# Kernel tuning notes

Measured on AMD Instinct MI355X. Metric: run time of the kernel, lower is better.

## Reference

```python
import jax, jax.numpy as jnp
import numpy as np

B, S, H = 2, 2048, 2048
NH, HD = 16, 128
I = 8192
EPS = float(np.finfo(np.float32).eps)  # torch RMSNorm default eps=None -> dtype eps


def rmsnorm(x, w):
    var = jnp.mean(jnp.square(x), axis=-1, keepdims=True)
    return x * jax.lax.rsqrt(var + EPS) * w


def setup_inputs() -> dict:
    key = jax.random.key(0)
    ks = jax.random.split(key, 8)
    s = 0.02
    return {
        "hidden_states": jax.random.normal(ks[0], (B, S, H), jnp.float32),
        "Wq": jax.random.normal(ks[1], (H, H), jnp.float32) * s,
        "Wk": jax.random.normal(ks[2], (H, H), jnp.float32) * s,
        "Wv": jax.random.normal(ks[3], (H, H), jnp.float32) * s,
        "Wo": jax.random.normal(ks[4], (H, H), jnp.float32) * s,
        "Wg": jax.random.normal(ks[5], (I, H), jnp.float32) * s,
        "Wu": jax.random.normal(ks[6], (I, H), jnp.float32) * s,
        "Wd": jax.random.normal(ks[7], (H, I), jnp.float32) * s,
        "g_in": jnp.ones((H,), jnp.float32),
        "g_post": jnp.ones((H,), jnp.float32),
    }


def reference(hidden_states, Wq, Wk, Wv, Wo, Wg, Wu, Wd, g_in, g_post):
    residual = hidden_states
    x = rmsnorm(hidden_states, g_in)
    # projections: nn.Linear does x @ W.T
    q = (x @ Wq.T).reshape(B, S, NH, HD).transpose(0, 2, 1, 3)  # [B,NH,S,HD]
    k = (x @ Wk.T).reshape(B, S, NH, HD).transpose(0, 2, 1, 3)
    v = (x @ Wv.T).reshape(B, S, NH, HD).transpose(0, 2, 1, 3)
    scores = jnp.einsum("bhqd,bhkd->bhqk", q, k) / jnp.sqrt(jnp.float32(HD))
    attn = jax.nn.softmax(scores, axis=-1)
    out = jnp.einsum("bhqk,bhkd->bhqd", attn, v)
    out = out.transpose(0, 2, 1, 3).reshape(B, S, H)
    hidden_states = residual + out @ Wo.T
    residual = hidden_states
    x = rmsnorm(hidden_states, g_post)
    mlp = (jax.nn.silu(x @ Wg.T) * (x @ Wu.T)) @ Wd.T
    return residual + mlp
```

## Files before the change

### kernel.cpp

```cpp
#include <hip/hip_runtime.h>

using u16 = unsigned short;
using u32 = unsigned int;

typedef __attribute__((ext_vector_type(8))) __bf16 bf16x8;
typedef __attribute__((ext_vector_type(4))) float f32x4;

__device__ __forceinline__ u16 f2bf(float f) {
  u32 u = __float_as_uint(f);
  u32 r = (u + 0x7fffu + ((u >> 16) & 1u)) >> 16;
  return (u16)r;
}
__device__ __forceinline__ u32 pk2(float a, float b) {
  return (u32)f2bf(a) | ((u32)f2bf(b) << 16);
}
__device__ __forceinline__ float bf2f(u16 h) {
  return __uint_as_float(((u32)h) << 16);
}
__device__ __forceinline__ void gload16(const u16* g, u16* l) {
  __builtin_amdgcn_global_load_lds((const __attribute__((address_space(1))) void*)g,
                                   (__attribute__((address_space(3))) void*)l, 16, 0, 0);
}
__device__ __forceinline__ f32x4 mfma_bf16(bf16x8 a, bf16x8 b, f32x4 c) {
  return __builtin_amdgcn_mfma_f32_16x16x32_bf16(a, b, c, 0, 0, 0);
}

__global__ __launch_bounds__(256) void cvt_bf16(const float* __restrict__ in,
                                                u16* __restrict__ out, int n8) {
  int i = blockIdx.x * 256 + threadIdx.x;
  int stride = gridDim.x * 256;
  for (; i < n8; i += stride) {
    float4 a = ((const float4*)in)[(size_t)i * 2];
    float4 b = ((const float4*)in)[(size_t)i * 2 + 1];
    ((uint4*)out)[i] = make_uint4(pk2(a.x, a.y), pk2(a.z, a.w), pk2(b.x, b.y), pk2(b.z, b.w));
  }
}

__global__ __launch_bounds__(256) void rmsnorm_bf16(const float* __restrict__ x,
                                                    const float* __restrict__ g,
                                                    u16* __restrict__ o) {
  const int row = blockIdx.x;
  const int tid = threadIdx.x;
  const float4* xr = (const float4*)(x + (size_t)row * 2048);
  float4 a = xr[tid * 2], b = xr[tid * 2 + 1];
  float s = a.x * a.x + a.y * a.y + a.z * a.z + a.w * a.w +
            b.x * b.x + b.y * b.y + b.z * b.z + b.w * b.w;
#pragma unroll
  for (int off = 1; off < 64; off <<= 1) s += __shfl_xor(s, off);
  __shared__ float red[4];
  if ((tid & 63) == 0) red[tid >> 6] = s;
  __syncthreads();
  s = red[0] + red[1] + red[2] + red[3];
  const float r = rsqrtf(s * (1.0f / 2048.0f) + 1.1920929e-07f);
  const float4* gr = (const float4*)g;
  float4 ga = gr[tid * 2], gb = gr[tid * 2 + 1];
  ((uint4*)(o + (size_t)row * 2048))[tid] =
      make_uint4(pk2(a.x * r * ga.x, a.y * r * ga.y), pk2(a.z * r * ga.z, a.w * r * ga.w),
                 pk2(b.x * r * gb.x, b.y * r * gb.y), pk2(b.z * r * gb.z, b.w * r * gb.w));
}

template <int EPI, int BN, int WM, int WN>
__global__ __launch_bounds__(512, 2) void gemm256(const u16* __restrict__ A,
                                                  const u16* __restrict__ B,
                                                  u16* Cb, float* Cf, const float* __restrict__ Res,
                                                  int M, int N, int K, int lda) {
  constexpr int NBH = BN / 128;
  constexpr int MR = 256 / WM / 16;
  constexpr int NR = BN / WN / 16;
  constexpr int HALF = 8192;
  alignas(16) __shared__ u16 lds[2][(2 + NBH) * HALF];

  const int tid = threadIdx.x;
  const int w = tid >> 6, lane = tid & 63;
  const int lo = lane & 15, hi = lane >> 4;

  const int nwg = gridDim.x;
  const int swz = (blockIdx.x & 7) * (nwg >> 3) + (blockIdx.x >> 3);
  const int nbx = N / BN;
  const int bm = (swz / nbx) * 256, bn = (swz % nbx) * BN;

  const int wm = w / WN, wn = w % WN;
  const int WRB = wm * (256 / WM), WCB = wn * (BN / WN);
  const int ah = WRB >> 7, arb = WRB & 127;
  const int bh = WCB >> 7, brb = WCB & 127;

  const int trow = tid >> 3, twin = tid & 7;
  const int scol = (twin ^ (trow & 7)) * 8;
  const u16* Ag = A + (size_t)(bm + trow) * lda + scol;
  const u16* Bg = B + (size_t)(bn + trow) * K + scol;

  f32x4 acc[MR][NR] = {};

#define STAGE(Ld, kt)                                                              \
  {                                                                                \
    _Pragma("unroll") for (int hc = 0; hc < 4; ++hc)                               \
        gload16(Ag + (size_t)(hc * 64) * lda + (kt), (Ld) + hc * 4096 + tid * 8);  \
    _Pragma("unroll") for (int hc = 0; hc < NBH * 2; ++hc)                         \
        gload16(Bg + (size_t)(hc * 64) * K + (kt), (Ld) + (2 + 0) * HALF + hc * 4096 + tid * 8); \
  }

  STAGE(&lds[0][0], 0);
  __syncthreads();
  int cur = 0;
  for (int kt = 0; kt < K; kt += 64) {
    if (kt + 64 < K) STAGE(&lds[cur ^ 1][0], kt + 64);
    const u16* LA = &lds[cur][0] + ah * HALF;
    const u16* LB = &lds[cur][0] + (2 + bh) * HALF;
#pragma unroll
    for (int ks = 0; ks < 2; ++ks) {
      const int pw = ((ks << 2) | hi) ^ (lo & 7);
      bf16x8 af[MR], bf[NR];
#pragma unroll
      for (int m = 0; m < MR; ++m)
        af[m] = *(const bf16x8*)(LA + (arb + m * 16 + lo) * 64 + pw * 8);
#pragma unroll
      for (int n = 0; n < NR; ++n)
        bf[n] = *(const bf16x8*)(LB + (brb + n * 16 + lo) * 64 + pw * 8);
      __builtin_amdgcn_s_setprio(1);
#pragma unroll
      for (int m = 0; m < MR; ++m)
#pragma unroll
        for (int n = 0; n < NR; ++n) acc[m][n] = mfma_bf16(af[m], bf[n], acc[m][n]);
      __builtin_amdgcn_s_setprio(0);
    }
    __syncthreads();
    cur ^= 1;
  }
#undef STAGE

#pragma unroll
  for (int m = 0; m < MR; ++m) {
    const int gr = bm + WRB + m * 16 + hi * 4;
#pragma unroll
    for (int n = 0; n < NR; ++n) {
      const int gc = bn + WCB + n * 16 + lo;
#pragma unroll
      for (int r = 0; r < 4; ++r) {
        const size_t idx = (size_t)(gr + r) * N + gc;
        if constexpr (EPI == 1) {
          Cf[idx] = Res[idx] + acc[m][n][r];
        } else if constexpr (EPI == 2) {
          float g = bf2f(Cb[idx]);
          float s = g / (1.f + __expf(-g));
          Cb[idx] = f2bf(s * acc[m][n][r]);
        } else {
          Cb[idx] = f2bf(acc[m][n][r]);
        }
      }
    }
  }
}

template <int EPI>
__global__ __launch_bounds__(256) void gemm_bt(const u16* __restrict__ A,
                                               const float* __restrict__ B,
                                               u16* Cb, float* Cf, const float* Res,
                                               int M, int N, int K) {
  alignas(16) __shared__ u16 As[128 * 32];
  alignas(16) __shared__ u16 Bs[128 * 32];
  const int tid = threadIdx.x;
  const int w = tid >> 6, lane = tid & 63;
  const int lo = lane & 15, hi = lane >> 4;
  const int bm = blockIdx.y * 128, bn = blockIdx.x * 128;
  const int wr = (w >> 1) * 64, wc = (w & 1) * 64;
  f32x4 acc[4][4] = {};
  const int r0 = tid >> 2, kc0 = (tid & 3) * 8;
  const u16* a0 = A + (size_t)(bm + r0) * K + kc0;
  const u16* a1 = A + (size_t)(bm + 64 + r0) * K + kc0;
  const float* b0 = B + (size_t)(bn + r0) * K + kc0;
  const float* b1 = B + (size_t)(bn + 64 + r0) * K + kc0;
  u16* asd0 = &As[(size_t)tid * 8];
  u16* asd1 = &As[(size_t)(tid + 256) * 8];
  u16* bsd0 = &Bs[(size_t)tid * 8];
  u16* bsd1 = &Bs[(size_t)(tid + 256) * 8];
  for (int kt = 0; kt < K; kt += 32) {
    gload16(a0 + kt, asd0);
    gload16(a1 + kt, asd1);
    float4 x0 = *(const float4*)(b0 + kt);
    float4 x1 = *(const float4*)(b0 + kt + 4);
    float4 y0 = *(const float4*)(b1 + kt);
    float4 y1 = *(const float4*)(b1 + kt + 4);
    *(uint4*)bsd0 = make_uint4(pk2(x0.x, x0.y), pk2(x0.z, x0.w), pk2(x1.x, x1.y), pk2(x1.z, x1.w));
    *(uint4*)bsd1 = make_uint4(pk2(y0.x, y0.y), pk2(y0.z, y0.w), pk2(y1.x, y1.y), pk2(y1.z, y1.w));
    __syncthreads();
    bf16x8 af[4], bfr[4];
#pragma unroll
    for (int i = 0; i < 4; ++i) {
      af[i] = *(const bf16x8*)(&As[(wr + i * 16 + lo) * 32 + hi * 8]);
      bfr[i] = *(const bf16x8*)(&Bs[(wc + i * 16 + lo) * 32 + hi * 8]);
    }
#pragma unroll
    for (int i = 0; i < 4; ++i)
#pragma unroll
      for (int j = 0; j < 4; ++j) acc[i][j] = mfma_bf16(af[i], bfr[j], acc[i][j]);
    __syncthreads();
  }
#pragma unroll
  for (int i = 0; i < 4; ++i) {
    const int gr = bm + wr + i * 16 + hi * 4;
#pragma unroll
    for (int j = 0; j < 4; ++j) {
      const int gc = bn + wc + j * 16 + lo;
#pragma unroll
      for (int r = 0; r < 4; ++r) {
        const size_t idx = (size_t)(gr + r) * N + gc;
        if constexpr (EPI == 1) {
          Cf[idx] = Res[idx] + acc[i][j][r];
        } else if constexpr (EPI == 2) {
          float g = bf2f(Cb[idx]);
          float s = g / (1.f + __expf(-g));
          Cb[idx] = f2bf(s * acc[i][j][r]);
        } else {
          Cb[idx] = f2bf(acc[i][j][r]);
        }
      }
    }
  }
}

__global__ __launch_bounds__(256) void transpose_v(const u16* __restrict__ v,
                                                   u16* __restrict__ vt, int ldv) {
  __shared__ u16 t[32][33];
  const int bh = blockIdx.z, b = bh >> 4, h = bh & 15;
  const int s0 = blockIdx.x * 32, d0 = blockIdx.y * 32;
  const int tx = threadIdx.x, ty = threadIdx.y;
#pragma unroll
  for (int i = 0; i < 4; ++i)
    t[ty + i * 8][tx] = v[(size_t)(b * 2048 + s0 + ty + i * 8) * ldv + h * 128 + d0 + tx];
  __syncthreads();
#pragma unroll
  for (int i = 0; i < 4; ++i)
    vt[(size_t)(bh * 128 + d0 + ty + i * 8) * 2048 + s0 + tx] = t[tx][ty + i * 8];
}

__global__ __launch_bounds__(256) void attn_fwd2(const u16* __restrict__ q,
                                                 const u16* __restrict__ k,
                                                 const u16* __restrict__ vt,
                                                 u16* o, int ldq) {
  constexpr int S = 2048;
  alignas(16) __shared__ u16 Ks[2][64 * 128];
  alignas(16) __shared__ u16 Vs[2][128 * 64];
  alignas(16) __shared__ u16 plds[4][16 * 72];
  const int bh = blockIdx.y, b = bh >> 4, h = bh & 15;
  const int tid = threadIdx.x, w = tid >> 6, lane = tid & 63;
  const int lo = lane & 15, hi = lane >> 4;
  const int qr = blockIdx.x * 64 + w * 16;
  u16* pl = &plds[w][0];

  bf16x8 qf[4];
  const u16* qb = q + (size_t)(b * S + qr + lo) * ldq + h * 128 + hi * 8;
#pragma unroll
  for (int ks = 0; ks < 4; ++ks) qf[ks] = *(const bf16x8*)(qb + ks * 32);

  f32x4 oacc[8] = {};
  float m[4], l[4];
#pragma unroll
  for (int r = 0; r < 4; ++r) { m[r] = -1e30f; l[r] = 0.f; }

  const u16* kb = k + (size_t)(b * S) * ldq + h * 128;
  const u16* vb = vt + (size_t)bh * 128 * S;

  const int kcs = ((((tid & 15) * 16) ^ (((tid >> 4) & 7) << 4)) >> 1);
  const int vcs = ((((tid & 7) * 16) ^ (((tid >> 3) & 7) << 4)) >> 1);
  const u16* kgs = kb + (size_t)(tid >> 4) * ldq + kcs;
  const u16* vgs = vb + (size_t)(tid >> 3) * S + vcs;

  int cur = 0;
#pragma unroll
  for (int c = 0; c < 4; ++c) gload16(kgs + (size_t)(c * 16) * ldq, &Ks[0][c * 2048 + tid * 8]);
#pragma unroll
  for (int c = 0; c < 4; ++c) gload16(vgs + (size_t)(c * 32) * S, &Vs[0][c * 2048 + tid * 8]);
  __syncthreads();

  const int swq = (lo & 7) << 4;

  for (int kv = 0; kv < S; kv += 64) {
    if (kv + 64 < S) {
      const int nb = cur ^ 1;
#pragma unroll
      for (int c = 0; c < 4; ++c)
        gload16(kgs + (size_t)(kv + 64 + c * 16) * ldq, &Ks[nb][c * 2048 + tid * 8]);
#pragma unroll
      for (int c = 0; c < 4; ++c)
        gload16(vgs + (size_t)(c * 32) * S + kv + 64, &Vs[nb][c * 2048 + tid * 8]);
    }
    const u16* Kc = &Ks[cur][0];
    const u16* Vc = &Vs[cur][0];

    f32x4 sacc[4] = {};
    __builtin_amdgcn_s_setprio(1);
#pragma unroll
    for (int ks = 0; ks < 4; ++ks)
#pragma unroll
      for (int n = 0; n < 4; ++n) {
        bf16x8 kf = *(const bf16x8*)(Kc + (n * 16 + lo) * 128 + (((ks * 64 + hi * 16) ^ swq) >> 1));
        sacc[n] = mfma_bf16(qf[ks], kf, sacc[n]);
      }
    __builtin_amdgcn_s_setprio(0);

    constexpr float sc = 0.08838834764831845f;
    constexpr float L2E = 1.4426950408889634f;
#pragma unroll
    for (int n = 0; n < 4; ++n) sacc[n] = sacc[n] * sc;
    float mv[4];
#pragma unroll
    for (int r = 0; r < 4; ++r)
      mv[r] = fmaxf(fmaxf(sacc[0][r], sacc[1][r]), fmaxf(sacc[2][r], sacc[3][r]));
#pragma unroll
    for (int off = 1; off < 16; off <<= 1)
#pragma unroll
      for (int r = 0; r < 4; ++r) mv[r] = fmaxf(mv[r], __shfl_xor(mv[r], off));
    float corr[4];
#pragma unroll
    for (int r = 0; r < 4; ++r) {
      float mn = fmaxf(m[r], mv[r]);
      corr[r] = exp2f((m[r] - mn) * L2E);
      m[r] = mn;
    }
    f32x4 p[4];
#pragma unroll
    for (int n = 0; n < 4; ++n)
#pragma unroll
      for (int r = 0; r < 4; ++r) p[n][r] = exp2f((sacc[n][r] - m[r]) * L2E);
    float ps[4];
#pragma unroll
    for (int r = 0; r < 4; ++r) ps[r] = p[0][r] + p[1][r] + p[2][r] + p[3][r];
#pragma unroll
    for (int off = 1; off < 16; off <<= 1)
#pragma unroll
      for (int r = 0; r < 4; ++r) ps[r] += __shfl_xor(ps[r], off);
#pragma unroll
    for (int r = 0; r < 4; ++r) l[r] = l[r] * corr[r] + ps[r];
#pragma unroll
    for (int f = 0; f < 8; ++f)
#pragma unroll
      for (int r = 0; r < 4; ++r) oacc[f][r] *= corr[r];

#pragma unroll
    for (int n = 0; n < 4; ++n)
#pragma unroll
      for (int r = 0; r < 4; ++r)
        pl[(hi * 4 + r) * 72 + n * 16 + lo] = f2bf(p[n][r]);
    asm volatile("s_waitcnt lgkmcnt(0)" ::: "memory");
    bf16x8 pf0 = *(const bf16x8*)(pl + lo * 72 + hi * 8);
    bf16x8 pf1 = *(const bf16x8*)(pl + lo * 72 + 32 + hi * 8);

    __builtin_amdgcn_s_setprio(1);
#pragma unroll
    for (int f = 0; f < 8; ++f) {
      const int row = f * 16 + lo;
      bf16x8 vf0 = *(const bf16x8*)(Vc + row * 64 + (((hi * 16) ^ swq) >> 1));
      bf16x8 vf1 = *(const bf16x8*)(Vc + row * 64 + (((64 + hi * 16) ^ swq) >> 1));
      oacc[f] = mfma_bf16(pf0, vf0, oacc[f]);
      oacc[f] = mfma_bf16(pf1, vf1, oacc[f]);
    }
    __builtin_amdgcn_s_setprio(0);

    __syncthreads();
    cur ^= 1;
  }

  u16* ob = o + (size_t)(b * S + qr) * ldq + h * 128;
#pragma unroll
  for (int f = 0; f < 8; ++f)
#pragma unroll
    for (int r = 0; r < 4; ++r)
      ob[(size_t)(hi * 4 + r) * ldq + f * 16 + lo] = f2bf(oacc[f][r] / l[r]);
}

extern "C" void kernel_launch(void* const* d_in, const int* in_sizes, int n_in,
                              void* d_out, int out_size, void* d_ws, size_t ws_size,
                              hipStream_t stream) {
  constexpr int B = 2, S = 2048, H = 2048, NH = 16, I = 8192;
  constexpr int M = B * S;

  const float* hs = (const float*)d_in[0];
  const float* Wq = (const float*)d_in[1];
  const float* Wk = (const float*)d_in[2];
  const float* Wv = (const float*)d_in[3];
  const float* Wo = (const float*)d_in[4];
  const float* Wg = (const float*)d_in[5];
  const float* Wu = (const float*)d_in[6];
  const float* Wd = (const float*)d_in[7];
  const float* g_in = (const float*)d_in[8];
  const float* g_post = (const float*)d_in[9];
  float* out = (float*)d_out;

  constexpr size_t SZ_HH = (size_t)H * H * 2;
  constexpr size_t SZ_IH = (size_t)I * H * 2;
  constexpr size_t SZ_MH = (size_t)M * H * 2;
  constexpr size_t NEED_NEW = SZ_MH + 3 * SZ_MH + SZ_MH + SZ_IH;

  if (ws_size >= NEED_NEW) {
    char* p = (char*)d_ws;
    u16* x_b = (u16*)p;    p += SZ_MH;
    u16* qkv_b = (u16*)p;  p += 3 * SZ_MH;
    u16* vt_b = (u16*)p;   p += SZ_MH;
    u16* wsc = (u16*)p;    p += SZ_IH;
    u16* gate_b = qkv_b;

    rmsnorm_bf16<<<M, 256, 0, stream>>>(hs, g_in, x_b);

    cvt_bf16<<<1024, 256, 0, stream>>>(Wq, wsc, H * H / 8);
    cvt_bf16<<<1024, 256, 0, stream>>>(Wk, wsc + (size_t)H * H, H * H / 8);
    cvt_bf16<<<1024, 256, 0, stream>>>(Wv, wsc + (size_t)2 * H * H, H * H / 8);
    gemm256<0, 256, 2, 4><<<(M / 256) * (3 * H / 256), 512, 0, stream>>>(
        x_b, wsc, qkv_b, nullptr, nullptr, M, 3 * H, H, H);

    transpose_v<<<dim3(S / 32, 128 / 32, B * NH), dim3(32, 8), 0, stream>>>(
        qkv_b + 2 * H, vt_b, 3 * H);
    attn_fwd2<<<dim3(S / 64, B * NH), 256, 0, stream>>>(qkv_b, qkv_b + H, vt_b, qkv_b, 3 * H);

    cvt_bf16<<<1024, 256, 0, stream>>>(Wo, wsc, H * H / 8);
    gemm256<1, 128, 4, 2><<<(M / 256) * (H / 128), 512, 0, stream>>>(
        qkv_b, wsc, nullptr, out, hs, M, H, H, 3 * H);

    rmsnorm_bf16<<<M, 256, 0, stream>>>(out, g_post, x_b);

    cvt_bf16<<<1024, 256, 0, stream>>>(Wg, wsc, I * H / 8);
    gemm256<0, 256, 2, 4><<<(M / 256) * (I / 256), 512, 0, stream>>>(
        x_b, wsc, gate_b, nullptr, nullptr, M, I, H, H);
    cvt_bf16<<<1024, 256, 0, stream>>>(Wu, wsc, I * H / 8);
    gemm256<2, 256, 2, 4><<<(M / 256) * (I / 256), 512, 0, stream>>>(
        x_b, wsc, gate_b, nullptr, nullptr, M, I, H, H);
    cvt_bf16<<<1024, 256, 0, stream>>>(Wd, wsc, I * H / 8);
    gemm256<1, 128, 4, 2><<<(M / 256) * (H / 128), 512, 0, stream>>>(
        gate_b, wsc, nullptr, out, out, M, H, I, I);
    return;
  }

  constexpr int MC = 2048;
  char* p = (char*)d_ws;
  u16* x_b = (u16*)p;   p += SZ_MH;
  u16* q_b = (u16*)p;   p += SZ_MH;
  u16* k_b = (u16*)p;   p += SZ_MH;
  u16* v_b = (u16*)p;   p += SZ_MH;
  u16* vt_b = (u16*)p;  p += SZ_MH;
  u16* g_mlp = k_b;

  rmsnorm_bf16<<<M, 256, 0, stream>>>(hs, g_in, x_b);
  const dim3 gHH(H / 128, M / 128);
  gemm_bt<0><<<gHH, 256, 0, stream>>>(x_b, Wq, q_b, nullptr, nullptr, M, H, H);
  gemm_bt<0><<<gHH, 256, 0, stream>>>(x_b, Wk, k_b, nullptr, nullptr, M, H, H);
  gemm_bt<0><<<gHH, 256, 0, stream>>>(x_b, Wv, v_b, nullptr, nullptr, M, H, H);
  transpose_v<<<dim3(S / 32, 128 / 32, B * NH), dim3(32, 8), 0, stream>>>(v_b, vt_b, H);
  attn_fwd2<<<dim3(S / 64, B * NH), 256, 0, stream>>>(q_b, k_b, vt_b, q_b, H);
  gemm_bt<1><<<gHH, 256, 0, stream>>>(q_b, Wo, nullptr, out, hs, M, H, H);
  rmsnorm_bf16<<<M, 256, 0, stream>>>(out, g_post, x_b);
  const dim3 gIH(I / 128, MC / 128), gHI(H / 128, MC / 128);
  for (int mc = 0; mc < M / MC; ++mc) {
    const u16* xc = x_b + (size_t)mc * MC * H;
    float* oc = out + (size_t)mc * MC * H;
    gemm_bt<0><<<gIH, 256, 0, stream>>>(xc, Wg, g_mlp, nullptr, nullptr, MC, I, H);
    gemm_bt<2><<<gIH, 256, 0, stream>>>(xc, Wu, g_mlp, nullptr, nullptr, MC, I, H);
    gemm_bt<1><<<gHI, 256, 0, stream>>>(g_mlp, Wd, nullptr, oc, oc, MC, H, I);
  }
}
```

Before: 871.0 us.

## Triple-buffer GEMM pipeline, XCD-aware tile mapping, lazy softmax rescale in attention

```diff
diff --git a/kernel.cpp b/kernel.cpp
--- a/kernel.cpp
+++ b/kernel.cpp
@@ -7,9 +7,8 @@
 typedef __attribute__((ext_vector_type(4))) float f32x4;
 
 __device__ __forceinline__ u16 f2bf(float f) {
-  u32 u = __float_as_uint(f);
-  u32 r = (u + 0x7fffu + ((u >> 16) & 1u)) >> 16;
-  return (u16)r;
+  __bf16 h = (__bf16)f;
+  return __builtin_bit_cast(u16, h);
 }
 __device__ __forceinline__ u32 pk2(float a, float b) {
   return (u32)f2bf(a) | ((u32)f2bf(b) << 16);
@@ -59,92 +58,101 @@
                  pk2(b.x * r * gb.x, b.y * r * gb.y), pk2(b.z * r * gb.z, b.w * r * gb.w));
 }
 
-template <int EPI, int BN, int WM, int WN>
-__global__ __launch_bounds__(512, 2) void gemm256(const u16* __restrict__ A,
-                                                  const u16* __restrict__ B,
-                                                  u16* Cb, float* Cf, const float* __restrict__ Res,
-                                                  int M, int N, int K, int lda) {
-  constexpr int NBH = BN / 128;
-  constexpr int MR = 256 / WM / 16;
-  constexpr int NR = BN / WN / 16;
-  constexpr int HALF = 8192;
-  alignas(16) __shared__ u16 lds[2][(2 + NBH) * HALF];
-
+template <int EPI>
+__global__ __launch_bounds__(512, 1) void gemm3b(const u16* __restrict__ A,
+                                                 const u16* __restrict__ B,
+                                                 u16* Cb, float* Cf,
+                                                 const float* __restrict__ Res,
+                                                 int M, int N, int K, int lda) {
+  constexpr int BUF = 24576;
+  alignas(16) __shared__ u16 lds[3 * BUF];
   const int tid = threadIdx.x;
   const int w = tid >> 6, lane = tid & 63;
   const int lo = lane & 15, hi = lane >> 4;
 
-  const int nwg = gridDim.x;
-  const int swz = (blockIdx.x & 7) * (nwg >> 3) + (blockIdx.x >> 3);
-  const int nbx = N / BN;
-  const int bm = (swz / nbx) * 256, bn = (swz % nbx) * BN;
-
-  const int wm = w / WN, wn = w % WN;
-  const int WRB = wm * (256 / WM), WCB = wn * (BN / WN);
-  const int ah = WRB >> 7, arb = WRB & 127;
-  const int bh = WCB >> 7, brb = WCB & 127;
-
-  const int trow = tid >> 3, twin = tid & 7;
-  const int scol = (twin ^ (trow & 7)) * 8;
-  const u16* Ag = A + (size_t)(bm + trow) * lda + scol;
-  const u16* Bg = B + (size_t)(bn + trow) * K + scol;
-
-  f32x4 acc[MR][NR] = {};
-
-#define STAGE(Ld, kt)                                                              \
-  {                                                                                \
-    _Pragma("unroll") for (int hc = 0; hc < 4; ++hc)                               \
-        gload16(Ag + (size_t)(hc * 64) * lda + (kt), (Ld) + hc * 4096 + tid * 8);  \
-    _Pragma("unroll") for (int hc = 0; hc < NBH * 2; ++hc)                         \
-        gload16(Bg + (size_t)(hc * 64) * K + (kt), (Ld) + (2 + 0) * HALF + hc * 4096 + tid * 8); \
-  }
-
-  STAGE(&lds[0][0], 0);
-  __syncthreads();
+  const int nbm = M >> 8, nbx = N >> 7;
+  const int RM = nbm >> 1, RN = nbx >> 2;
+  const int xcd = blockIdx.x & 7, idx = blockIdx.x >> 3;
+  const int bm = ((xcd >> 2) * RM + idx / RN) << 8;
+  const int bn = ((xcd & 3) * RN + idx % RN) << 7;
+
+  const int wm = w >> 1, wn = w & 1;
+
+  const int scol = ((tid & 7) ^ ((tid >> 3) & 7)) * 8;
+  const u16* Ag = A + (size_t)(bm + (tid >> 3)) * lda + scol;
+  const u16* Bg = B + (size_t)(bn + (tid >> 3)) * K + scol;
+
+  f32x4 acc[4][4] = {};
+
+#define STG(b, kt)                                                                    \
+  {                                                                                   \
+    _Pragma("unroll") for (int c = 0; c < 4; ++c)                                     \
+        gload16(Ag + (size_t)(c * 64) * lda + (kt), &lds[(b)*BUF + c * 4096 + tid * 8]); \
+    _Pragma("unroll") for (int c = 0; c < 2; ++c)                                     \
+        gload16(Bg + (size_t)(c * 64) * K + (kt), &lds[(b)*BUF + 16384 + c * 4096 + tid * 8]); \
+  }
+
+  const int NT = K >> 6;
+  STG(0, 0);
+  STG(1, 64);
+
   int cur = 0;
-  for (int kt = 0; kt < K; kt += 64) {
-    if (kt + 64 < K) STAGE(&lds[cur ^ 1][0], kt + 64);
-    const u16* LA = &lds[cur][0] + ah * HALF;
-    const u16* LB = &lds[cur][0] + (2 + bh) * HALF;
+  for (int T = 0; T < NT; ++T) {
+    if (T + 1 < NT) {
+      asm volatile("s_waitcnt vmcnt(6)" ::: "memory");
+    } else {
+      asm volatile("s_waitcnt vmcnt(0)" ::: "memory");
+    }
+    __builtin_amdgcn_s_barrier();
+    __builtin_amdgcn_sched_barrier(0);
+
+    const u16* LA = &lds[cur * BUF];
+    const u16* LB = LA + 16384;
+    bf16x8 af[4][2], bf[4][2];
 #pragma unroll
     for (int ks = 0; ks < 2; ++ks) {
-      const int pw = ((ks << 2) | hi) ^ (lo & 7);
-      bf16x8 af[MR], bf[NR];
-#pragma unroll
-      for (int m = 0; m < MR; ++m)
-        af[m] = *(const bf16x8*)(LA + (arb + m * 16 + lo) * 64 + pw * 8);
-#pragma unroll
-      for (int n = 0; n < NR; ++n)
-        bf[n] = *(const bf16x8*)(LB + (brb + n * 16 + lo) * 64 + pw * 8);
-      __builtin_amdgcn_s_setprio(1);
-#pragma unroll
-      for (int m = 0; m < MR; ++m)
-#pragma unroll
-        for (int n = 0; n < NR; ++n) acc[m][n] = mfma_bf16(af[m], bf[n], acc[m][n]);
-      __builtin_amdgcn_s_setprio(0);
-    }
-    __syncthreads();
-    cur ^= 1;
-  }
-#undef STAGE
-
-#pragma unroll
-  for (int m = 0; m < MR; ++m) {
-    const int gr = bm + WRB + m * 16 + hi * 4;
-#pragma unroll
-    for (int n = 0; n < NR; ++n) {
-      const int gc = bn + WCB + n * 16 + lo;
+#pragma unroll
+      for (int m = 0; m < 4; ++m)
+        af[m][ks] = *(const bf16x8*)(LA + (wm * 64 + m * 16 + lo) * 64 +
+                                     ((ks * 4 + hi) ^ (lo & 7)) * 8);
+#pragma unroll
+      for (int n = 0; n < 4; ++n)
+        bf[n][ks] = *(const bf16x8*)(LB + (wn * 64 + n * 16 + lo) * 64 +
+                                     ((ks * 4 + hi) ^ (lo & 7)) * 8);
+    }
+    if (T + 2 < NT) {
+      const int nb = (cur + 2) % 3;
+      STG(nb, (T + 2) << 6);
+    }
+    __builtin_amdgcn_s_setprio(1);
+#pragma unroll
+    for (int ks = 0; ks < 2; ++ks)
+#pragma unroll
+      for (int m = 0; m < 4; ++m)
+#pragma unroll
+        for (int n = 0; n < 4; ++n) acc[m][n] = mfma_bf16(af[m][ks], bf[n][ks], acc[m][n]);
+    __builtin_amdgcn_s_setprio(0);
+    cur = (cur + 1) % 3;
+  }
+#undef STG
+
+#pragma unroll
+  for (int m = 0; m < 4; ++m) {
+    const int gr = bm + wm * 64 + m * 16 + hi * 4;
+#pragma unroll
+    for (int n = 0; n < 4; ++n) {
+      const int gc = bn + wn * 64 + n * 16 + lo;
 #pragma unroll
       for (int r = 0; r < 4; ++r) {
-        const size_t idx = (size_t)(gr + r) * N + gc;
+        const size_t idx2 = (size_t)(gr + r) * N + gc;
         if constexpr (EPI == 1) {
-          Cf[idx] = Res[idx] + acc[m][n][r];
+          Cf[idx2] = Res[idx2] + acc[m][n][r];
         } else if constexpr (EPI == 2) {
-          float g = bf2f(Cb[idx]);
+          float g = bf2f(Cb[idx2]);
           float s = g / (1.f + __expf(-g));
-          Cb[idx] = f2bf(s * acc[m][n][r]);
+          Cb[idx2] = f2bf(s * acc[m][n][r]);
         } else {
-          Cb[idx] = f2bf(acc[m][n][r]);
+          Cb[idx2] = f2bf(acc[m][n][r]);
         }
       }
     }
@@ -273,6 +281,7 @@
   __syncthreads();
 
   const int swq = (lo & 7) << 4;
+  constexpr float SCL = 0.12752956f;
 
   for (int kv = 0; kv < S; kv += 64) {
     if (kv + 64 < S) {
@@ -298,10 +307,6 @@
       }
     __builtin_amdgcn_s_setprio(0);
 
-    constexpr float sc = 0.08838834764831845f;
-    constexpr float L2E = 1.4426950408889634f;
-#pragma unroll
-    for (int n = 0; n < 4; ++n) sacc[n] = sacc[n] * sc;
     float mv[4];
 #pragma unroll
     for (int r = 0; r < 4; ++r)
@@ -310,31 +315,39 @@
     for (int off = 1; off < 16; off <<= 1)
 #pragma unroll
       for (int r = 0; r < 4; ++r) mv[r] = fmaxf(mv[r], __shfl_xor(mv[r], off));
-    float corr[4];
-#pragma unroll
-    for (int r = 0; r < 4; ++r) {
-      float mn = fmaxf(m[r], mv[r]);
-      corr[r] = exp2f((m[r] - mn) * L2E);
-      m[r] = mn;
-    }
+
+    bool need = false;
+#pragma unroll
+    for (int r = 0; r < 4; ++r) need = need || (mv[r] > m[r] + 62.f);
+    if (__any(need)) {
+#pragma unroll
+      for (int r = 0; r < 4; ++r) {
+        float nm = fmaxf(m[r], mv[r]);
+        float c = exp2f((m[r] - nm) * SCL);
+        m[r] = nm;
+        l[r] *= c;
+#pragma unroll
+        for (int f = 0; f < 8; ++f) oacc[f][r] *= c;
+      }
+    }
+    float mm[4];
+#pragma unroll
+    for (int r = 0; r < 4; ++r) mm[r] = m[r] * SCL;
+
     f32x4 p[4];
 #pragma unroll
     for (int n = 0; n < 4; ++n)
 #pragma unroll
-      for (int r = 0; r < 4; ++r) p[n][r] = exp2f((sacc[n][r] - m[r]) * L2E);
+      for (int r = 0; r < 4; ++r) p[n][r] = exp2f(fmaf(sacc[n][r], SCL, -mm[r]));
     float ps[4];
 #pragma unroll
-    for (int r = 0; r < 4; ++r) ps[r] = p[0][r] + p[1][r] + p[2][r] + p[3][r];
+    for (int r = 0; r < 4; ++r) ps[r] = (p[0][r] + p[1][r]) + (p[2][r] + p[3][r]);
 #pragma unroll
     for (int off = 1; off < 16; off <<= 1)
 #pragma unroll
       for (int r = 0; r < 4; ++r) ps[r] += __shfl_xor(ps[r], off);
 #pragma unroll
-    for (int r = 0; r < 4; ++r) l[r] = l[r] * corr[r] + ps[r];
-#pragma unroll
-    for (int f = 0; f < 8; ++f)
-#pragma unroll
-      for (int r = 0; r < 4; ++r) oacc[f][r] *= corr[r];
+    for (int r = 0; r < 4; ++r) l[r] += ps[r];
 
 #pragma unroll
     for (int n = 0; n < 4; ++n)
@@ -404,7 +417,7 @@
     cvt_bf16<<<1024, 256, 0, stream>>>(Wq, wsc, H * H / 8);
     cvt_bf16<<<1024, 256, 0, stream>>>(Wk, wsc + (size_t)H * H, H * H / 8);
     cvt_bf16<<<1024, 256, 0, stream>>>(Wv, wsc + (size_t)2 * H * H, H * H / 8);
-    gemm256<0, 256, 2, 4><<<(M / 256) * (3 * H / 256), 512, 0, stream>>>(
+    gemm3b<0><<<(M / 256) * (3 * H / 128), 512, 0, stream>>>(
         x_b, wsc, qkv_b, nullptr, nullptr, M, 3 * H, H, H);
 
     transpose_v<<<dim3(S / 32, 128 / 32, B * NH), dim3(32, 8), 0, stream>>>(
@@ -412,19 +425,19 @@
     attn_fwd2<<<dim3(S / 64, B * NH), 256, 0, stream>>>(qkv_b, qkv_b + H, vt_b, qkv_b, 3 * H);
 
     cvt_bf16<<<1024, 256, 0, stream>>>(Wo, wsc, H * H / 8);
-    gemm256<1, 128, 4, 2><<<(M / 256) * (H / 128), 512, 0, stream>>>(
+    gemm3b<1><<<(M / 256) * (H / 128), 512, 0, stream>>>(
         qkv_b, wsc, nullptr, out, hs, M, H, H, 3 * H);
 
     rmsnorm_bf16<<<M, 256, 0, stream>>>(out, g_post, x_b);
 
     cvt_bf16<<<1024, 256, 0, stream>>>(Wg, wsc, I * H / 8);
-    gemm256<0, 256, 2, 4><<<(M / 256) * (I / 256), 512, 0, stream>>>(
+    gemm3b<0><<<(M / 256) * (I / 128), 512, 0, stream>>>(
         x_b, wsc, gate_b, nullptr, nullptr, M, I, H, H);
     cvt_bf16<<<1024, 256, 0, stream>>>(Wu, wsc, I * H / 8);
-    gemm256<2, 256, 2, 4><<<(M / 256) * (I / 256), 512, 0, stream>>>(
+    gemm3b<2><<<(M / 256) * (I / 128), 512, 0, stream>>>(
         x_b, wsc, gate_b, nullptr, nullptr, M, I, H, H);
     cvt_bf16<<<1024, 256, 0, stream>>>(Wd, wsc, I * H / 8);
-    gemm256<1, 128, 4, 2><<<(M / 256) * (H / 128), 512, 0, stream>>>(
+    gemm3b<1><<<(M / 256) * (H / 128), 512, 0, stream>>>(
         gate_b, wsc, nullptr, out, out, M, H, I, I);
     return;
   }
```

After: 855.0 us. Within noise of the previous version (-1.8%).
